# Optimization experiments

Measured on AMD Instinct MI355X. Metric: run time of the kernel, lower is better.

Reference implementation:

```python
import jax, jax.numpy as jnp
import numpy as np

B, S, D, H = 1, 2048, 2048, 16
HD = D // H  # head_dim = 128
EPS = 1e-6


def setup_inputs() -> dict:
    key = jax.random.key(0)
    ks = jax.random.split(key, 12)
    sc = 0.02
    x = jax.random.normal(ks[0], (B, S, D), jnp.float32)
    wq = jax.random.normal(ks[1], (D, D), jnp.float32) * sc
    bq = jnp.zeros((D,), jnp.float32)
    wk = jax.random.normal(ks[2], (D, D), jnp.float32) * sc
    bk = jnp.zeros((D,), jnp.float32)
    wv = jax.random.normal(ks[3], (D, D), jnp.float32) * sc
    bv = jnp.zeros((D,), jnp.float32)
    wo = jax.random.normal(ks[4], (D, D), jnp.float32) * sc
    bo = jnp.zeros((D,), jnp.float32)
    gq = jnp.ones((D,), jnp.float32)  # RMSNorm weight for q
    gk = jnp.ones((D,), jnp.float32)  # RMSNorm weight for k
    # Rotary frequency table: complex freqs = cos + i*sin, shape [S, 1, HD//2]
    pos = jnp.arange(S, dtype=jnp.float32)
    inv = 1.0 / (10000.0 ** (jnp.arange(0, HD, 2, dtype=jnp.float32) / HD))  # [HD//2]
    theta = pos[:, None] * inv[None, :]  # [S, HD//2]
    freqs_cos = jnp.cos(theta)[:, None, :]  # [S, 1, HD//2]
    freqs_sin = jnp.sin(theta)[:, None, :]
    return {"x": x, "wq": wq, "bq": bq, "wk": wk, "bk": bk, "wv": wv, "bv": bv,
            "wo": wo, "bo": bo, "gq": gq, "gk": gk,
            "freqs_cos": freqs_cos, "freqs_sin": freqs_sin}


def _rmsnorm(x, g):
    # RMSNorm over full model dim (applied BEFORE head split, as in source)
    return x * jax.lax.rsqrt(jnp.mean(x * x, axis=-1, keepdims=True) + EPS) * g


def _rope(x, cos, sin):
    # x: [B,S,D] -> (B,S,H,HD//2,2) complex pairs; complex mult by (cos + i sin)
    b, s, d = x.shape
    xr = x.reshape(b, s, H, HD // 2, 2)
    a, bb = xr[..., 0], xr[..., 1]
    # cos/sin [S,1,HD//2] broadcast against [B,S,H,HD//2]
    ra = a * cos - bb * sin
    rb = a * sin + bb * cos
    return jnp.stack([ra, rb], axis=-1).reshape(b, s, d)


def reference(x, wq, bq, wk, bk, wv, bv, wo, bo, gq, gk, freqs_cos, freqs_sin):
    b, s, d = x.shape
    q = _rope(_rmsnorm(x @ wq.T + bq, gq), freqs_cos, freqs_sin)
    k = _rope(_rmsnorm(x @ wk.T + bk, gk), freqs_cos, freqs_sin)
    v = x @ wv.T + bv
    qh = q.reshape(b, s, H, HD).transpose(0, 2, 1, 3)  # [B,H,S,HD]
    kh = k.reshape(b, s, H, HD).transpose(0, 2, 1, 3)
    vh = v.reshape(b, s, H, HD).transpose(0, 2, 1, 3)
    scores = jnp.einsum('bhqd,bhkd->bhqk', qh, kh) / np.sqrt(HD).astype(np.float32)
    attn = jax.nn.softmax(scores, axis=-1)
    out = jnp.einsum('bhqk,bhkd->bhqd', attn, vh)
    out = out.transpose(0, 2, 1, 3).reshape(b, s, d)
    return out @ wo.T + bo
```

## Files before the change

kernel.cpp:

```cpp
#include <hip/hip_runtime.h>
#include <math.h>

typedef unsigned short u16;
typedef unsigned int u32;
typedef __bf16 bf16x8 __attribute__((ext_vector_type(8)));
typedef float f32x4 __attribute__((ext_vector_type(4)));
typedef float f32x16 __attribute__((ext_vector_type(16)));

__device__ __forceinline__ u16 f2bf(float f) {
  unsigned u = __float_as_uint(f);
  u += 0x7fff + ((u >> 16) & 1);
  return (u16)(u >> 16);
}

__device__ __forceinline__ float b2f(u16 x) {
  return __uint_as_float((u32)x << 16);
}

__device__ __forceinline__ u32 cvtpk(float lo, float hi) {
  u32 r;
  asm("v_cvt_pk_bf16_f32 %0, %1, %2" : "=v"(r) : "v"(lo), "v"(hi));
  return r;
}

__device__ __forceinline__ void pswap(u32& x, u32& y) {
  asm volatile("v_permlane32_swap_b32 %0, %1" : "+v"(x), "+v"(y));
}

__device__ __forceinline__ void gload_lds16(const void* g, void* l) {
  __builtin_amdgcn_global_load_lds(
      (const __attribute__((address_space(1))) unsigned int*)g,
      (__attribute__((address_space(3))) unsigned int*)l, 16, 0, 0);
}

__global__ __launch_bounds__(256) void k_cvt5(const float* __restrict__ s0,
                                              const float* __restrict__ s1,
                                              const float* __restrict__ s2,
                                              const float* __restrict__ s3,
                                              const float* __restrict__ s4,
                                              u16* __restrict__ dx,
                                              u16* __restrict__ dqkv,
                                              u16* __restrict__ dwo) {
  const int y = blockIdx.y;
  const float* s = (y == 0) ? s0 : (y == 1) ? s1 : (y == 2) ? s2
                   : (y == 3) ? s3 : s4;
  u16* d = (y == 0) ? dx : (y == 4) ? dwo : dqkv + (size_t)(y - 1) * 4194304;
  int i = (blockIdx.x * 256 + threadIdx.x) * 4;
  float4 v = *(const float4*)(s + i);
  ushort4 o;
  o.x = f2bf(v.x); o.y = f2bf(v.y); o.z = f2bf(v.z); o.w = f2bf(v.w);
  *(ushort4*)(d + i) = o;
}

__global__ __launch_bounds__(512, 4) void k_gemm_big(const u16* __restrict__ A,
                                                     const u16* __restrict__ B,
                                                     u16* __restrict__ C,
                                                     int M, int N, int K) {
  __shared__ __align__(16) char lds[2][40960];
  const int tid = threadIdx.x;
  const int wid = tid >> 6, lane = tid & 63;
  const int lr = lane & 15, lg = lane >> 4;
  const int wm = (wid >> 2) * 64, wn = (wid & 3) * 48;
  const int nbx = N / 192, nby = M >> 7;
  const int colsPerXcd = nbx >> 3;
  const int xcd = blockIdx.x & 7, idx = blockIdx.x >> 3;
  const int bx = xcd * colsPerXcd + idx / nby;
  const int by = idx % nby;
  const int bm = by * 128, bn = bx * 192;
  const int srow = tid >> 3;
  const int schunk = (tid & 7) ^ (srow & 7);
  const size_t rsK = (size_t)K * 2;
  const char* gA = (const char*)A + (size_t)(bm + srow) * rsK + schunk * 16;
  const char* gB = (const char*)B + (size_t)(bn + srow) * rsK + schunk * 16;
  char* dA = (char*)lds + wid * 1024;
  char* dB = (char*)lds + 16384 + wid * 1024;

#define STAGE(cur, k0)                                                         \
  {                                                                            \
    _Pragma("unroll") for (int i = 0; i < 2; ++i)                              \
        gload_lds16(gA + (size_t)(i * 64) * rsK + (size_t)(k0) * 2,            \
                    dA + (cur) * 40960 + i * 8192);                            \
    _Pragma("unroll") for (int i = 0; i < 3; ++i)                              \
        gload_lds16(gB + (size_t)(i * 64) * rsK + (size_t)(k0) * 2,            \
                    dB + (cur) * 40960 + i * 8192);                            \
  }

  f32x4 acc[4][3] = {};
  STAGE(0, 0);
  STAGE(1, 64);
  asm volatile("s_waitcnt vmcnt(5)" ::: "memory");
  __builtin_amdgcn_s_barrier();
  const int NT = K >> 6;
  int cur = 0;
  const int rsw = (lr & 7);
  for (int t = 0; t < NT; ++t) {
    const char* La = (const char*)lds + cur * 40960;
    const char* Lb = La + 16384;
    bf16x8 af[4][2], bfr[3][2];
#pragma unroll
    for (int mi = 0; mi < 4; ++mi)
#pragma unroll
      for (int kk = 0; kk < 2; ++kk)
        af[mi][kk] = *(const bf16x8*)(La + (wm + mi * 16 + lr) * 128 +
                                      (((kk * 4 + lg) ^ rsw) * 16));
#pragma unroll
    for (int ni = 0; ni < 3; ++ni)
#pragma unroll
      for (int kk = 0; kk < 2; ++kk)
        bfr[ni][kk] = *(const bf16x8*)(Lb + (wn + ni * 16 + lr) * 128 +
                                       (((kk * 4 + lg) ^ rsw) * 16));
    asm volatile("s_waitcnt lgkmcnt(0)" ::: "memory");
    __builtin_amdgcn_s_barrier();
    if (t + 2 < NT) STAGE(cur, (t + 2) << 6);
    __builtin_amdgcn_s_setprio(1);
#pragma unroll
    for (int kk = 0; kk < 2; ++kk)
#pragma unroll
      for (int mi = 0; mi < 4; ++mi)
#pragma unroll
        for (int ni = 0; ni < 3; ++ni)
          acc[mi][ni] = __builtin_amdgcn_mfma_f32_16x16x32_bf16(
              af[mi][kk], bfr[ni][kk], acc[mi][ni], 0, 0, 0);
    __builtin_amdgcn_s_setprio(0);
    if (t + 2 < NT)
      asm volatile("s_waitcnt vmcnt(5)" ::: "memory");
    else
      asm volatile("s_waitcnt vmcnt(0)" ::: "memory");
    __builtin_amdgcn_s_barrier();
    cur ^= 1;
  }
#undef STAGE
#pragma unroll
  for (int mi = 0; mi < 4; ++mi)
#pragma unroll
    for (int ni = 0; ni < 3; ++ni)
#pragma unroll
      for (int j = 0; j < 4; ++j)
        C[(size_t)(bm + wm + mi * 16 + lg * 4 + j) * N + bn + wn + ni * 16 + lr] =
            f2bf(acc[mi][ni][j]);
}

__global__ __launch_bounds__(256, 2) void k_gemm_pipe(const u16* __restrict__ A,
                                                      const u16* __restrict__ B,
                                                      const float* __restrict__ bias,
                                                      float* __restrict__ C,
                                                      int M, int N, int K) {
  __shared__ __align__(16) char lds[2][24576];
  const int tid = threadIdx.x;
  const int wid = tid >> 6, lane = tid & 63;
  const int lr = lane & 15, lg = lane >> 4;
  const int wm = (wid >> 1) * 64, wn = (wid & 1) * 32;
  const int nbx = N >> 6, nby = M >> 7;
  const int colsPerXcd = nbx >> 3;
  const int xcd = blockIdx.x & 7, idx = blockIdx.x >> 3;
  const int bx = xcd * colsPerXcd + idx / nby;
  const int by = idx % nby;
  const int bm = by * 128, bn = bx * 64;
  const int srow = tid >> 3;
  const int schunk = (tid & 7) ^ (srow & 7);
  const size_t rsK = (size_t)K * 2;
  const char* gA = (const char*)A + (size_t)(bm + srow) * rsK + schunk * 16;
  const char* gB = (const char*)B + (size_t)(bn + srow) * rsK + schunk * 16;
  char* dA = (char*)lds + wid * 1024;
  char* dB = (char*)lds + 16384 + wid * 1024;

#define STAGE(cur, k0)                                                         \
  {                                                                            \
    _Pragma("unroll") for (int i = 0; i < 4; ++i)                              \
        gload_lds16(gA + (size_t)(i * 32) * rsK + (size_t)(k0) * 2,            \
                    dA + (cur) * 24576 + i * 4096);                            \
    _Pragma("unroll") for (int i = 0; i < 2; ++i)                              \
        gload_lds16(gB + (size_t)(i * 32) * rsK + (size_t)(k0) * 2,            \
                    dB + (cur) * 24576 + i * 4096);                            \
  }

  f32x4 acc[4][2] = {};
  STAGE(0, 0);
  STAGE(1, 64);
  asm volatile("s_waitcnt vmcnt(6)" ::: "memory");
  __builtin_amdgcn_s_barrier();
  const int NT = K >> 6;
  int cur = 0;
  const int rsw = (lr & 7);
  for (int t = 0; t < NT; ++t) {
    const char* La = (const char*)lds + cur * 24576;
    const char* Lb = La + 16384;
    bf16x8 af[4][2], bfr[2][2];
#pragma unroll
    for (int mi = 0; mi < 4; ++mi)
#pragma unroll
      for (int kk = 0; kk < 2; ++kk)
        af[mi][kk] = *(const bf16x8*)(La + (wm + mi * 16 + lr) * 128 +
                                      (((kk * 4 + lg) ^ rsw) * 16));
#pragma unroll
    for (int ni = 0; ni < 2; ++ni)
#pragma unroll
      for (int kk = 0; kk < 2; ++kk)
        bfr[ni][kk] = *(const bf16x8*)(Lb + (wn + ni * 16 + lr) * 128 +
                                       (((kk * 4 + lg) ^ rsw) * 16));
    asm volatile("s_waitcnt lgkmcnt(0)" ::: "memory");
    __builtin_amdgcn_s_barrier();
    if (t + 2 < NT) STAGE(cur, (t + 2) << 6);
    __builtin_amdgcn_s_setprio(1);
#pragma unroll
    for (int kk = 0; kk < 2; ++kk)
#pragma unroll
      for (int mi = 0; mi < 4; ++mi)
#pragma unroll
        for (int ni = 0; ni < 2; ++ni)
          acc[mi][ni] = __builtin_amdgcn_mfma_f32_16x16x32_bf16(
              af[mi][kk], bfr[ni][kk], acc[mi][ni], 0, 0, 0);
    __builtin_amdgcn_s_setprio(0);
    if (t + 2 < NT)
      asm volatile("s_waitcnt vmcnt(6)" ::: "memory");
    else
      asm volatile("s_waitcnt vmcnt(0)" ::: "memory");
    __builtin_amdgcn_s_barrier();
    cur ^= 1;
  }
#undef STAGE
#pragma unroll
  for (int mi = 0; mi < 4; ++mi)
#pragma unroll
    for (int ni = 0; ni < 2; ++ni) {
      int col = bn + wn + ni * 16 + lr;
      float bb = bias[col];
#pragma unroll
      for (int j = 0; j < 4; ++j)
        C[(size_t)(bm + wm + mi * 16 + lg * 4 + j) * N + col] =
            acc[mi][ni][j] + bb;
    }
}

__global__ __launch_bounds__(256) void k_rmsnorm_rope(
    const u16* __restrict__ qkv, const float* __restrict__ bq,
    const float* __restrict__ bk, const float* __restrict__ gq,
    const float* __restrict__ gk, const float* __restrict__ fcos,
    const float* __restrict__ fsin, u16* __restrict__ qb, u16* __restrict__ kb) {
  const int s = blockIdx.x, which = blockIdx.y;
  const int t = threadIdx.x;
  const u16* src = qkv + (size_t)s * 6144 + which * 2048;
  const float* bias = which ? bk : bq;
  const float* g = which ? gk : gq;
  u16* dst = (which ? kb : qb) + (size_t)s * 2048;
  const int c0 = t * 8;
  uint4 raw = *(const uint4*)(src + c0);
  const u16* rp = (const u16*)&raw;
  float4 b0 = *(const float4*)(bias + c0);
  float4 b1 = *(const float4*)(bias + c0 + 4);
  float v[8];
  v[0] = b2f(rp[0]) + b0.x; v[1] = b2f(rp[1]) + b0.y;
  v[2] = b2f(rp[2]) + b0.z; v[3] = b2f(rp[3]) + b0.w;
  v[4] = b2f(rp[4]) + b1.x; v[5] = b2f(rp[5]) + b1.y;
  v[6] = b2f(rp[6]) + b1.z; v[7] = b2f(rp[7]) + b1.w;
  float ss = 0.f;
#pragma unroll
  for (int j = 0; j < 8; ++j) ss += v[j] * v[j];
#pragma unroll
  for (int m = 1; m < 64; m <<= 1) ss += __shfl_xor(ss, m);
  __shared__ float red[4];
  if ((t & 63) == 0) red[t >> 6] = ss;
  __syncthreads();
  float r = rsqrtf((red[0] + red[1] + red[2] + red[3]) * (1.0f / 2048.0f) + 1e-6f);
  if (!which) r *= 0.08838834764831843f * 1.4426950408889634f;
  float4 g0 = *(const float4*)(g + c0);
  float4 g1 = *(const float4*)(g + c0 + 4);
  float gg[8] = {g0.x, g0.y, g0.z, g0.w, g1.x, g1.y, g1.z, g1.w};
  const int p0 = (c0 & 127) >> 1;
  u16 o[8];
#pragma unroll
  for (int j = 0; j < 4; ++j) {
    float a = v[2 * j] * r * gg[2 * j];
    float b = v[2 * j + 1] * r * gg[2 * j + 1];
    float co = fcos[s * 64 + p0 + j], si = fsin[s * 64 + p0 + j];
    o[2 * j]     = f2bf(a * co - b * si);
    o[2 * j + 1] = f2bf(a * si + b * co);
  }
  ushort4 q0; q0.x = o[0]; q0.y = o[1]; q0.z = o[2]; q0.w = o[3];
  ushort4 q1; q1.x = o[4]; q1.y = o[5]; q1.z = o[6]; q1.w = o[7];
  *(ushort4*)(dst + c0) = q0;
  *(ushort4*)(dst + c0 + 4) = q1;
}

__global__ __launch_bounds__(256) void k_transpose_v(const u16* __restrict__ qkv,
                                                     const float* __restrict__ bv,
                                                     u16* __restrict__ vT) {
  __shared__ float tile[64][65];
  const int s0 = blockIdx.x * 64, d0 = blockIdx.y * 64;
  const int t = threadIdx.x;
  const int tc = (t & 15) * 4, tr = t >> 4;
  float4 bb = *(const float4*)(bv + d0 + tc);
#pragma unroll
  for (int i = 0; i < 4; ++i) {
    int sr = tr + i * 16;
    ushort4 x = *(const ushort4*)(qkv + (size_t)(s0 + sr) * 6144 + 4096 + d0 + tc);
    tile[sr][tc + 0] = b2f(x.x) + bb.x;
    tile[sr][tc + 1] = b2f(x.y) + bb.y;
    tile[sr][tc + 2] = b2f(x.z) + bb.z;
    tile[sr][tc + 3] = b2f(x.w) + bb.w;
  }
  __syncthreads();
#pragma unroll
  for (int i = 0; i < 4; ++i) {
    int dr = tr + i * 16;
    ushort4 o;
    o.x = f2bf(tile[tc + 0][dr]);
    o.y = f2bf(tile[tc + 1][dr]);
    o.z = f2bf(tile[tc + 2][dr]);
    o.w = f2bf(tile[tc + 3][dr]);
    *(ushort4*)(vT + (size_t)(d0 + dr) * 2048 + s0 + tc) = o;
  }
}

__global__ __launch_bounds__(256, 2) void k_attn(const u16* __restrict__ qb,
                                                 const u16* __restrict__ kb,
                                                 const u16* __restrict__ vT,
                                                 float* __restrict__ opart,
                                                 float* __restrict__ ml) {
  __shared__ __align__(16) char Ks[2][16384];
  __shared__ __align__(16) char Vs[2][16384];
  const int bid = blockIdx.x;
  const int xcd = bid & 7, j = bid >> 3;
  const int h = xcd * 2 + (j & 1);
  const int qt = (j >> 1) & 15;
  const int ks = j >> 5;
  const int tid = threadIdx.x;
  const int wid = tid >> 6, lane = tid & 63;
  const int l31 = lane & 31, hi = lane >> 5;
  const int q0w = qt * 128 + wid * 32;
  const char* kbB = (const char*)kb;
  const char* vTB = (const char*)vT;
  const int krow = tid >> 4;
  const int kc = (tid & 15) ^ krow;
  const int vrow = tid >> 3;
  const int vc = (tid & 7) ^ (vrow & 7);

#define STAGE(buf, k0)                                                         \
  {                                                                            \
    _Pragma("unroll") for (int i = 0; i < 4; ++i)                              \
        gload_lds16(kbB + (size_t)((k0) + i * 16 + krow) * 4096 + h * 256 +    \
                        kc * 16,                                               \
                    (char*)Ks + (buf) * 16384 + i * 4096 + wid * 1024);        \
    _Pragma("unroll") for (int i = 0; i < 4; ++i)                              \
        gload_lds16(vTB + (size_t)(h * 128 + i * 32 + vrow) * 4096 +           \
                        (size_t)(k0) * 2 + vc * 16,                            \
                    (char*)Vs + (buf) * 16384 + i * 4096 + wid * 1024);        \
  }

  bf16x8 qf[8];
#pragma unroll
  for (int ds = 0; ds < 8; ++ds)
    qf[ds] = *(const bf16x8*)(qb + (size_t)(q0w + l31) * 2048 + h * 128 +
                              ds * 16 + hi * 8);
  f32x16 o[4] = {};
  f32x16 o4 = {};
  float mrun = -3.0e38f;
  const int kbeg = ks * 1024;
  const int ksw = l31 & 15, vsw = l31 & 7;
  union { u32 w[4]; bf16x8 v; } onesu;
  onesu.w[0] = 0x3F803F80u; onesu.w[1] = 0x3F803F80u;
  onesu.w[2] = 0x3F803F80u; onesu.w[3] = 0x3F803F80u;
  const bf16x8 vones = onesu.v;
  STAGE(0, kbeg);
  __syncthreads();
  int cur = 0;
  for (int t = 0; t < 16; ++t) {
    if (t + 1 < 16) STAGE(cur ^ 1, kbeg + (t + 1) * 64);
    const char* Kc = Ks[cur];
    const char* Vc = Vs[cur];
    f32x16 p0 = {}, p1 = {};
    __builtin_amdgcn_s_setprio(1);
#pragma unroll
    for (int ds = 0; ds < 8; ++ds) {
      bf16x8 kf0 = *(const bf16x8*)(Kc + l31 * 256 + (((ds * 2 + hi) ^ ksw) * 16));
      p0 = __builtin_amdgcn_mfma_f32_32x32x16_bf16(kf0, qf[ds], p0, 0, 0, 0);
      bf16x8 kf1 = *(const bf16x8*)(Kc + (32 + l31) * 256 +
                                    (((ds * 2 + hi) ^ ksw) * 16));
      p1 = __builtin_amdgcn_mfma_f32_32x32x16_bf16(kf1, qf[ds], p1, 0, 0, 0);
    }
    __builtin_amdgcn_s_setprio(0);
    {
      float tm[8];
#pragma unroll
      for (int r = 0; r < 8; ++r)
        tm[r] = fmaxf(fmaxf(p0[2 * r], p0[2 * r + 1]),
                      fmaxf(p1[2 * r], p1[2 * r + 1]));
#pragma unroll
      for (int s = 4; s > 0; s >>= 1)
#pragma unroll
        for (int r = 0; r < s; ++r) tm[r] = fmaxf(tm[r], tm[r + s]);
      float pm = fmaxf(tm[0], __shfl_xor(tm[0], 32));
      if (!__all(pm <= mrun + 8.0f)) {
        float nm = fmaxf(mrun, pm);
        float fv = __builtin_amdgcn_exp2f(mrun - nm);
#pragma unroll
        for (int dt = 0; dt < 4; ++dt) o[dt] *= fv;
        o4 *= fv;
        mrun = nm;
      }
    }
#pragma unroll
    for (int r = 0; r < 16; ++r) p0[r] = __builtin_amdgcn_exp2f(p0[r] - mrun);
#pragma unroll
    for (int r = 0; r < 16; ++r) p1[r] = __builtin_amdgcn_exp2f(p1[r] - mrun);
    bf16x8 pa[4];
#pragma unroll
    for (int sl = 0; sl < 2; ++sl) {
      u32 E0 = cvtpk(p0[8 * sl + 0], p0[8 * sl + 1]);
      u32 E1 = cvtpk(p0[8 * sl + 2], p0[8 * sl + 3]);
      u32 O0 = cvtpk(p0[8 * sl + 4], p0[8 * sl + 5]);
      u32 O1 = cvtpk(p0[8 * sl + 6], p0[8 * sl + 7]);
      pswap(E0, O0); pswap(E1, O1);
      union { u32 w[4]; bf16x8 v; } uu;
      uu.w[0] = E0; uu.w[1] = E1; uu.w[2] = O0; uu.w[3] = O1;
      pa[sl] = uu.v;
    }
#pragma unroll
    for (int sl = 0; sl < 2; ++sl) {
      u32 E0 = cvtpk(p1[8 * sl + 0], p1[8 * sl + 1]);
      u32 E1 = cvtpk(p1[8 * sl + 2], p1[8 * sl + 3]);
      u32 O0 = cvtpk(p1[8 * sl + 4], p1[8 * sl + 5]);
      u32 O1 = cvtpk(p1[8 * sl + 6], p1[8 * sl + 7]);
      pswap(E0, O0); pswap(E1, O1);
      union { u32 w[4]; bf16x8 v; } uu;
      uu.w[0] = E0; uu.w[1] = E1; uu.w[2] = O0; uu.w[3] = O1;
      pa[2 + sl] = uu.v;
    }
    __builtin_amdgcn_s_setprio(1);
#pragma unroll
    for (int s = 0; s < 4; ++s) {
#pragma unroll
      for (int dt = 0; dt < 4; ++dt) {
        bf16x8 vf = *(const bf16x8*)(Vc + (dt * 32 + l31) * 128 +
                                     (((s * 2 + hi) ^ vsw) * 16));
        o[dt] = __builtin_amdgcn_mfma_f32_32x32x16_bf16(pa[s], vf, o[dt], 0, 0, 0);
      }
      o4 = __builtin_amdgcn_mfma_f32_32x32x16_bf16(pa[s], vones, o4, 0, 0, 0);
    }
    __builtin_amdgcn_s_setprio(0);
    __syncthreads();
    cur ^= 1;
  }
#undef STAGE
  float* opb = opart + ((size_t)ks * 32768 + (size_t)h * 2048 + q0w) * 128 + l31;
#pragma unroll
  for (int dt = 0; dt < 4; ++dt)
#pragma unroll
    for (int r = 0; r < 16; ++r)
      opb[(size_t)((r & 3) + 8 * (r >> 2) + 4 * hi) * 128 + dt * 32] = o[dt][r];
  {
    const int rsel = (l31 & 3) | (((l31 >> 3) & 3) << 2);
    float cand = o4[0];
#pragma unroll
    for (int r = 1; r < 16; ++r) cand = (rsel == r) ? o4[r] : cand;
    float other = __shfl_xor(cand, 32);
    float lsum_q = (hi == ((l31 >> 2) & 1)) ? cand : other;
    if (lane < 32) {
      float2 v2; v2.x = mrun; v2.y = lsum_q;
      *(float2*)(ml + ((size_t)ks * 32768 + (size_t)h * 2048 + q0w + l31) * 2) = v2;
    }
  }
}

__global__ __launch_bounds__(256) void k_attn_merge(const float* __restrict__ opart,
                                                    const float* __restrict__ ml,
                                                    u16* __restrict__ ob) {
  const int r = blockIdx.x * 8 + (threadIdx.x >> 5);
  const int d0 = (threadIdx.x & 31) * 4;
  float2 ml0 = *(const float2*)(ml + (size_t)r * 2);
  float2 ml1 = *(const float2*)(ml + (size_t)(32768 + r) * 2);
  float M = fmaxf(ml0.x, ml1.x);
  float f0 = __builtin_amdgcn_exp2f(ml0.x - M);
  float f1 = __builtin_amdgcn_exp2f(ml1.x - M);
  float inv = 1.0f / (ml0.y * f0 + ml1.y * f1);
  float4 a = *(const float4*)(opart + (size_t)r * 128 + d0);
  float4 b = *(const float4*)(opart + (size_t)(32768 + r) * 128 + d0);
  int h = r >> 11, q = r & 2047;
  ushort4 o;
  o.x = f2bf((a.x * f0 + b.x * f1) * inv);
  o.y = f2bf((a.y * f0 + b.y * f1) * inv);
  o.z = f2bf((a.z * f0 + b.z * f1) * inv);
  o.w = f2bf((a.w * f0 + b.w * f1) * inv);
  *(ushort4*)(ob + (size_t)q * 2048 + h * 128 + d0) = o;
}

extern "C" void kernel_launch(void* const* d_in, const int* in_sizes, int n_in,
                              void* d_out, int out_size, void* d_ws, size_t ws_size,
                              hipStream_t stream) {
  const float* x    = (const float*)d_in[0];
  const float* wq   = (const float*)d_in[1];
  const float* bq   = (const float*)d_in[2];
  const float* wk   = (const float*)d_in[3];
  const float* bk   = (const float*)d_in[4];
  const float* wv   = (const float*)d_in[5];
  const float* bv   = (const float*)d_in[6];
  const float* wo   = (const float*)d_in[7];
  const float* bo   = (const float*)d_in[8];
  const float* gq   = (const float*)d_in[9];
  const float* gk   = (const float*)d_in[10];
  const float* fcos = (const float*)d_in[11];
  const float* fsin = (const float*)d_in[12];

  char* ws = (char*)d_ws;
  u16* qkv_pre = (u16*)ws;
  float* opart = (float*)ws;
  float* ml    = (float*)(ws + 33554432);
  u16* xb   = (u16*)(ws + 50331648);
  u16* wqkv = (u16*)(ws + 58720256);
  u16* qb   = (u16*)(ws + 50331648);
  u16* kb   = (u16*)(ws + 58720256);
  u16* vT   = (u16*)(ws + 67108864);
  u16* ao   = (u16*)(ws + 75497472);
  u16* wob  = (u16*)(ws + 83886080);

  k_cvt5<<<dim3(4096, 5), 256, 0, stream>>>(x, wq, wk, wv, wo, xb, wqkv, wob);

  k_gemm_big<<<512, 512, 0, stream>>>(xb, wqkv, qkv_pre, 2048, 6144, 2048);
  k_rmsnorm_rope<<<dim3(2048, 2), 256, 0, stream>>>(qkv_pre, bq, bk, gq, gk,
                                                    fcos, fsin, qb, kb);
  k_transpose_v<<<dim3(32, 32), 256, 0, stream>>>(qkv_pre, bv, vT);
  k_attn<<<512, 256, 0, stream>>>(qb, kb, vT, opart, ml);
  k_attn_merge<<<4096, 256, 0, stream>>>(opart, ml, ao);
  k_gemm_pipe<<<dim3(512), 256, 0, stream>>>(ao, wob, bo, (float*)d_out,
                                             2048, 2048, 2048);
}
```

Measured before the change: 156.5 us.

## Fuse split-K attention merge into attention kernel and split GEMM LDS reads

```diff
diff --git a/kernel.cpp b/kernel.cpp
--- a/kernel.cpp
+++ b/kernel.cpp
@@ -50,6 +50,10 @@
   ushort4 o;
   o.x = f2bf(v.x); o.y = f2bf(v.y); o.z = f2bf(v.z); o.w = f2bf(v.w);
   *(ushort4*)(d + i) = o;
+}
+
+__global__ __launch_bounds__(256) void k_zero(int* __restrict__ cnt) {
+  cnt[threadIdx.x] = 0;
 }
 
 __global__ __launch_bounds__(512, 4) void k_gemm_big(const u16* __restrict__ A,
@@ -96,31 +100,45 @@
   for (int t = 0; t < NT; ++t) {
     const char* La = (const char*)lds + cur * 40960;
     const char* Lb = La + 16384;
-    bf16x8 af[4][2], bfr[3][2];
-#pragma unroll
-    for (int mi = 0; mi < 4; ++mi)
-#pragma unroll
-      for (int kk = 0; kk < 2; ++kk)
-        af[mi][kk] = *(const bf16x8*)(La + (wm + mi * 16 + lr) * 128 +
-                                      (((kk * 4 + lg) ^ rsw) * 16));
+    bf16x8 af0[4], bf0[3], af1[4], bf1[3];
+#pragma unroll
+    for (int mi = 0; mi < 4; ++mi)
+      af0[mi] = *(const bf16x8*)(La + (wm + mi * 16 + lr) * 128 +
+                                 ((lg ^ rsw) * 16));
 #pragma unroll
     for (int ni = 0; ni < 3; ++ni)
-#pragma unroll
-      for (int kk = 0; kk < 2; ++kk)
-        bfr[ni][kk] = *(const bf16x8*)(Lb + (wn + ni * 16 + lr) * 128 +
-                                       (((kk * 4 + lg) ^ rsw) * 16));
+      bf0[ni] = *(const bf16x8*)(Lb + (wn + ni * 16 + lr) * 128 +
+                                 ((lg ^ rsw) * 16));
+    __builtin_amdgcn_sched_barrier(0);
+#pragma unroll
+    for (int mi = 0; mi < 4; ++mi)
+      af1[mi] = *(const bf16x8*)(La + (wm + mi * 16 + lr) * 128 +
+                                 (((4 + lg) ^ rsw) * 16));
+#pragma unroll
+    for (int ni = 0; ni < 3; ++ni)
+      bf1[ni] = *(const bf16x8*)(Lb + (wn + ni * 16 + lr) * 128 +
+                                 (((4 + lg) ^ rsw) * 16));
+    asm volatile("s_waitcnt lgkmcnt(7)" ::: "memory");
+    __builtin_amdgcn_sched_barrier(0);
+    __builtin_amdgcn_s_setprio(1);
+#pragma unroll
+    for (int mi = 0; mi < 4; ++mi)
+#pragma unroll
+      for (int ni = 0; ni < 3; ++ni)
+        acc[mi][ni] = __builtin_amdgcn_mfma_f32_16x16x32_bf16(
+            af0[mi], bf0[ni], acc[mi][ni], 0, 0, 0);
+    __builtin_amdgcn_s_setprio(0);
     asm volatile("s_waitcnt lgkmcnt(0)" ::: "memory");
+    __builtin_amdgcn_sched_barrier(0);
     __builtin_amdgcn_s_barrier();
     if (t + 2 < NT) STAGE(cur, (t + 2) << 6);
     __builtin_amdgcn_s_setprio(1);
 #pragma unroll
-    for (int kk = 0; kk < 2; ++kk)
-#pragma unroll
-      for (int mi = 0; mi < 4; ++mi)
-#pragma unroll
-        for (int ni = 0; ni < 3; ++ni)
-          acc[mi][ni] = __builtin_amdgcn_mfma_f32_16x16x32_bf16(
-              af[mi][kk], bfr[ni][kk], acc[mi][ni], 0, 0, 0);
+    for (int mi = 0; mi < 4; ++mi)
+#pragma unroll
+      for (int ni = 0; ni < 3; ++ni)
+        acc[mi][ni] = __builtin_amdgcn_mfma_f32_16x16x32_bf16(
+            af1[mi], bf1[ni], acc[mi][ni], 0, 0, 0);
     __builtin_amdgcn_s_setprio(0);
     if (t + 2 < NT)
       asm volatile("s_waitcnt vmcnt(5)" ::: "memory");
@@ -185,31 +203,45 @@
   for (int t = 0; t < NT; ++t) {
     const char* La = (const char*)lds + cur * 24576;
     const char* Lb = La + 16384;
-    bf16x8 af[4][2], bfr[2][2];
-#pragma unroll
-    for (int mi = 0; mi < 4; ++mi)
-#pragma unroll
-      for (int kk = 0; kk < 2; ++kk)
-        af[mi][kk] = *(const bf16x8*)(La + (wm + mi * 16 + lr) * 128 +
-                                      (((kk * 4 + lg) ^ rsw) * 16));
+    bf16x8 af0[4], bf0[2], af1[4], bf1[2];
+#pragma unroll
+    for (int mi = 0; mi < 4; ++mi)
+      af0[mi] = *(const bf16x8*)(La + (wm + mi * 16 + lr) * 128 +
+                                 ((lg ^ rsw) * 16));
 #pragma unroll
     for (int ni = 0; ni < 2; ++ni)
-#pragma unroll
-      for (int kk = 0; kk < 2; ++kk)
-        bfr[ni][kk] = *(const bf16x8*)(Lb + (wn + ni * 16 + lr) * 128 +
-                                       (((kk * 4 + lg) ^ rsw) * 16));
+      bf0[ni] = *(const bf16x8*)(Lb + (wn + ni * 16 + lr) * 128 +
+                                 ((lg ^ rsw) * 16));
+    __builtin_amdgcn_sched_barrier(0);
+#pragma unroll
+    for (int mi = 0; mi < 4; ++mi)
+      af1[mi] = *(const bf16x8*)(La + (wm + mi * 16 + lr) * 128 +
+                                 (((4 + lg) ^ rsw) * 16));
+#pragma unroll
+    for (int ni = 0; ni < 2; ++ni)
+      bf1[ni] = *(const bf16x8*)(Lb + (wn + ni * 16 + lr) * 128 +
+                                 (((4 + lg) ^ rsw) * 16));
+    asm volatile("s_waitcnt lgkmcnt(6)" ::: "memory");
+    __builtin_amdgcn_sched_barrier(0);
+    __builtin_amdgcn_s_setprio(1);
+#pragma unroll
+    for (int mi = 0; mi < 4; ++mi)
+#pragma unroll
+      for (int ni = 0; ni < 2; ++ni)
+        acc[mi][ni] = __builtin_amdgcn_mfma_f32_16x16x32_bf16(
+            af0[mi], bf0[ni], acc[mi][ni], 0, 0, 0);
+    __builtin_amdgcn_s_setprio(0);
     asm volatile("s_waitcnt lgkmcnt(0)" ::: "memory");
+    __builtin_amdgcn_sched_barrier(0);
     __builtin_amdgcn_s_barrier();
     if (t + 2 < NT) STAGE(cur, (t + 2) << 6);
     __builtin_amdgcn_s_setprio(1);
 #pragma unroll
-    for (int kk = 0; kk < 2; ++kk)
-#pragma unroll
-      for (int mi = 0; mi < 4; ++mi)
-#pragma unroll
-        for (int ni = 0; ni < 2; ++ni)
-          acc[mi][ni] = __builtin_amdgcn_mfma_f32_16x16x32_bf16(
-              af[mi][kk], bfr[ni][kk], acc[mi][ni], 0, 0, 0);
+    for (int mi = 0; mi < 4; ++mi)
+#pragma unroll
+      for (int ni = 0; ni < 2; ++ni)
+        acc[mi][ni] = __builtin_amdgcn_mfma_f32_16x16x32_bf16(
+            af1[mi], bf1[ni], acc[mi][ni], 0, 0, 0);
     __builtin_amdgcn_s_setprio(0);
     if (t + 2 < NT)
       asm volatile("s_waitcnt vmcnt(6)" ::: "memory");
@@ -316,7 +348,9 @@
                                                  const u16* __restrict__ kb,
                                                  const u16* __restrict__ vT,
                                                  float* __restrict__ opart,
-                                                 float* __restrict__ ml) {
+                                                 float2* __restrict__ ml,
+                                                 int* __restrict__ cnt,
+                                                 u16* __restrict__ ao) {
   __shared__ __align__(16) char Ks[2][16384];
   __shared__ __align__(16) char Vs[2][16384];
   const int bid = blockIdx.x;
@@ -324,6 +358,7 @@
   const int h = xcd * 2 + (j & 1);
   const int qt = (j >> 1) & 15;
   const int ks = j >> 5;
+  const int pair = h * 16 + qt;
   const int tid = threadIdx.x;
   const int wid = tid >> 6, lane = tid & 63;
   const int l31 = lane & 31, hi = lane >> 5;
@@ -442,46 +477,64 @@
     cur ^= 1;
   }
 #undef STAGE
-  float* opb = opart + ((size_t)ks * 32768 + (size_t)h * 2048 + q0w) * 128 + l31;
-#pragma unroll
-  for (int dt = 0; dt < 4; ++dt)
-#pragma unroll
-    for (int r = 0; r < 16; ++r)
-      opb[(size_t)((r & 3) + 8 * (r >> 2) + 4 * hi) * 128 + dt * 32] = o[dt][r];
+  float lsum_q;
   {
     const int rsel = (l31 & 3) | (((l31 >> 3) & 3) << 2);
     float cand = o4[0];
 #pragma unroll
     for (int r = 1; r < 16; ++r) cand = (rsel == r) ? o4[r] : cand;
     float other = __shfl_xor(cand, 32);
-    float lsum_q = (hi == ((l31 >> 2) & 1)) ? cand : other;
-    if (lane < 32) {
-      float2 v2; v2.x = mrun; v2.y = lsum_q;
-      *(float2*)(ml + ((size_t)ks * 32768 + (size_t)h * 2048 + q0w + l31) * 2) = v2;
-    }
-  }
-}
-
-__global__ __launch_bounds__(256) void k_attn_merge(const float* __restrict__ opart,
-                                                    const float* __restrict__ ml,
-                                                    u16* __restrict__ ob) {
-  const int r = blockIdx.x * 8 + (threadIdx.x >> 5);
-  const int d0 = (threadIdx.x & 31) * 4;
-  float2 ml0 = *(const float2*)(ml + (size_t)r * 2);
-  float2 ml1 = *(const float2*)(ml + (size_t)(32768 + r) * 2);
-  float M = fmaxf(ml0.x, ml1.x);
-  float f0 = __builtin_amdgcn_exp2f(ml0.x - M);
-  float f1 = __builtin_amdgcn_exp2f(ml1.x - M);
-  float inv = 1.0f / (ml0.y * f0 + ml1.y * f1);
-  float4 a = *(const float4*)(opart + (size_t)r * 128 + d0);
-  float4 b = *(const float4*)(opart + (size_t)(32768 + r) * 128 + d0);
-  int h = r >> 11, q = r & 2047;
-  ushort4 o;
-  o.x = f2bf((a.x * f0 + b.x * f1) * inv);
-  o.y = f2bf((a.y * f0 + b.y * f1) * inv);
-  o.z = f2bf((a.z * f0 + b.z * f1) * inv);
-  o.w = f2bf((a.w * f0 + b.w * f1) * inv);
-  *(ushort4*)(ob + (size_t)q * 2048 + h * 128 + d0) = o;
+    lsum_q = (hi == ((l31 >> 2) & 1)) ? cand : other;
+  }
+  float* op = opart + ((size_t)pair * 2 + ks) * 16384 + wid * 4096;
+#pragma unroll
+  for (int dt = 0; dt < 4; ++dt)
+#pragma unroll
+    for (int rr = 0; rr < 4; ++rr) {
+      f32x4 sl;
+      sl[0] = o[dt][rr * 4 + 0]; sl[1] = o[dt][rr * 4 + 1];
+      sl[2] = o[dt][rr * 4 + 2]; sl[3] = o[dt][rr * 4 + 3];
+      *(f32x4*)(op + (dt * 4 + rr) * 256 + lane * 4) = sl;
+    }
+  float2* mlp = ml + ((size_t)pair * 2 + ks) * 128 + wid * 32;
+  if (lane < 32) { float2 v2; v2.x = mrun; v2.y = lsum_q; mlp[l31] = v2; }
+  __threadfence();
+  __syncthreads();
+  __shared__ int who;
+  if (tid == 0) who = atomicAdd(&cnt[pair], 1);
+  __syncthreads();
+  if (who == 0) return;
+  __threadfence();
+  const int os = 1 - ks;
+  const float* oq = opart + ((size_t)pair * 2 + os) * 16384 + wid * 4096;
+  float2 mlB = (ml + ((size_t)pair * 2 + os) * 128 + wid * 32)[l31];
+  float fa[16], fb[16];
+#pragma unroll
+  for (int r = 0; r < 16; ++r) {
+    int src = (r & 3) + 8 * (r >> 2) + 4 * hi;
+    float mB = __shfl(mlB.x, src);
+    float lB = __shfl(mlB.y, src);
+    float mA = __shfl(mrun, src);
+    float lA = __shfl(lsum_q, src);
+    float M = fmaxf(mA, mB);
+    float eA = __builtin_amdgcn_exp2f(mA - M);
+    float eB = __builtin_amdgcn_exp2f(mB - M);
+    float inv = 1.0f / (lA * eA + lB * eB);
+    fa[r] = eA * inv; fb[r] = eB * inv;
+  }
+#pragma unroll
+  for (int dt = 0; dt < 4; ++dt) {
+    f32x4 bo[4];
+#pragma unroll
+    for (int rr = 0; rr < 4; ++rr)
+      bo[rr] = *(const f32x4*)(oq + (dt * 4 + rr) * 256 + lane * 4);
+#pragma unroll
+    for (int r = 0; r < 16; ++r) {
+      float val = o[dt][r] * fa[r] + bo[r >> 2][r & 3] * fb[r];
+      int qg = q0w + (r & 3) + 8 * (r >> 2) + 4 * hi;
+      ao[(size_t)qg * 2048 + h * 128 + dt * 32 + l31] = f2bf(val);
+    }
+  }
 }
 
 extern "C" void kernel_launch(void* const* d_in, const int* in_sizes, int n_in,
@@ -504,7 +557,8 @@
   char* ws = (char*)d_ws;
   u16* qkv_pre = (u16*)ws;
   float* opart = (float*)ws;
-  float* ml    = (float*)(ws + 33554432);
+  float2* ml   = (float2*)(ws + 33554432);
+  int* cnt     = (int*)(ws + 34078720);
   u16* xb   = (u16*)(ws + 50331648);
   u16* wqkv = (u16*)(ws + 58720256);
   u16* qb   = (u16*)(ws + 50331648);
@@ -514,13 +568,13 @@
   u16* wob  = (u16*)(ws + 83886080);
 
   k_cvt5<<<dim3(4096, 5), 256, 0, stream>>>(x, wq, wk, wv, wo, xb, wqkv, wob);
+  k_zero<<<1, 256, 0, stream>>>(cnt);
 
   k_gemm_big<<<512, 512, 0, stream>>>(xb, wqkv, qkv_pre, 2048, 6144, 2048);
   k_rmsnorm_rope<<<dim3(2048, 2), 256, 0, stream>>>(qkv_pre, bq, bk, gq, gk,
                                                     fcos, fsin, qb, kb);
   k_transpose_v<<<dim3(32, 32), 256, 0, stream>>>(qkv_pre, bv, vT);
-  k_attn<<<512, 256, 0, stream>>>(qb, kb, vT, opart, ml);
-  k_attn_merge<<<4096, 256, 0, stream>>>(opart, ml, ao);
+  k_attn<<<512, 256, 0, stream>>>(qb, kb, vT, opart, ml, cnt, ao);
   k_gemm_pipe<<<dim3(512), 256, 0, stream>>>(ao, wob, bo, (float*)d_out,
                                              2048, 2048, 2048);
 }
```

Result: slower. 246.3 us (+57.3%).
